# Kernel tuning notes

Hardware: AMD Instinct MI355X
Metric: run time of the kernel (lower is better)

## Reference

```python
import jax, jax.numpy as jnp
import numpy as np

K = 1024   # number of NNLS components (theta_1 is K x K)
B = 8192   # batched frames / columns


def setup_inputs() -> dict:
    key = jax.random.key(0)
    k1, k2, k3, k4 = jax.random.split(key, 4)
    # theta_1 = I - AtA / ||AtA||_F  -> near-identity contraction; emulate with
    # identity minus a small random symmetric-ish perturbation.
    pert = jax.random.normal(k1, (K, K), dtype=jnp.float32) * (1.0 / K)
    th1 = jnp.eye(K, dtype=jnp.float32) - pert
    Y = jax.random.uniform(k2, (K, B), dtype=jnp.float32)
    X_old = jax.random.uniform(k3, (K, B), dtype=jnp.float32)
    weight = jax.random.normal(k4, (K, B), dtype=jnp.float32) * 0.1  # theta_2 = Atb/n_AtA
    k = 2  # PGD iteration counter
    return {"th1": th1, "Y": Y, "X_old": X_old, "k": k, "weight": weight}


def reference(th1, Y, X_old, k, weight):
    # One projected-gradient-descent step of NNLS with Nesterov momentum:
    #   new_X = relu(th1 @ Y + weight)
    #   Y_new = new_X + (k-1)/(k+2) * (new_X - X_old)
    kf = jnp.float32(k)
    new_X = jax.nn.relu(jnp.matmul(th1, Y) + weight)          # [K, B]
    momentum = (kf - 1.0) / (kf + 2.0)
    Y_new = new_X + momentum * (new_X - X_old)                # [K, B]
    return (Y_new, new_X, k + 1, weight)
```

## Files before the change

### kernel.cpp

```cpp
#include <hip/hip_runtime.h>
#include <cstdint>


#define KDIM 1024
#define NDIM 8192
#define KB_ELEMS (1024UL * 8192UL)
#define LDA 40

typedef short short8 __attribute__((ext_vector_type(8)));
typedef float f32x4 __attribute__((ext_vector_type(4)));

struct __attribute__((aligned(4))) f4u { float x, y, z, w; };

__device__ __forceinline__ uint32_t pk2(float a, float b) {
  uint32_t ua = __builtin_bit_cast(uint32_t, a) + 0x8000u;
  uint32_t ub = __builtin_bit_cast(uint32_t, b) + 0x8000u;
  return (ua >> 16) | (ub & 0xFFFF0000u);
}

__global__ __launch_bounds__(512, 4) void nnls_gemm(
    const float* __restrict__ th1, const float* __restrict__ Y,
    const float* __restrict__ xold, const int* __restrict__ kin,
    const float* __restrict__ weight, float* __restrict__ out)
{
  __shared__ __align__(16) char smem[40960];
  unsigned short* As0 = (unsigned short*)smem;
  unsigned short* Bs0 = (unsigned short*)(smem + 10240);
  unsigned short* As1 = (unsigned short*)(smem + 20480);
  unsigned short* Bs1 = (unsigned short*)(smem + 30720);

  const int tid  = threadIdx.x;
  const int lane = tid & 63;
  const int w    = tid >> 6;
  const int wm = w >> 1, wn = w & 1;
  const int quad = lane >> 4, nl = lane & 15;

  const int m0 = blockIdx.y * 128;
  const int n0 = blockIdx.x * 128;

  const int ar = tid >> 3;
  const int ac = tid & 7;
  const float* abase = th1 + (size_t)(m0 + ar) * KDIM + ac * 4;

  const int bn = tid & 127;
  const int bk = (tid >> 7) * 8;
  const float* ybase = Y + (size_t)bk * NDIM + n0 + bn;

  float4 ab[2];
  float  yb[8];
  ab[0] = *(const float4*)(abase);
  ab[1] = *(const float4*)(abase + (size_t)64 * KDIM);
#pragma unroll
  for (int r = 0; r < 8; ++r) yb[r] = ybase[(size_t)r * NDIM];

  f32x4 acc[2][4] = {};

#pragma unroll 2
  for (int kt = 0; kt < 32; ++kt) {
    unsigned short* Asp = (kt & 1) ? As1 : As0;
    unsigned short* Bsp = (kt & 1) ? Bs1 : Bs0;

    {
      uint2 d0; d0.x = pk2(ab[0].x, ab[0].y); d0.y = pk2(ab[0].z, ab[0].w);
      *(uint2*)&Asp[ar * LDA + ac * 4] = d0;
      uint2 d1; d1.x = pk2(ab[1].x, ab[1].y); d1.y = pk2(ab[1].z, ab[1].w);
      *(uint2*)&Asp[(ar + 64) * LDA + ac * 4] = d1;
      uint4 e;
      e.x = pk2(yb[0], yb[1]); e.y = pk2(yb[2], yb[3]);
      e.z = pk2(yb[4], yb[5]); e.w = pk2(yb[6], yb[7]);
      *(uint4*)&Bsp[bn * LDA + bk] = e;
    }
    __syncthreads();

    if (kt < 31) {
      const float* an = abase + (kt + 1) * 32;
      ab[0] = *(const float4*)(an);
      ab[1] = *(const float4*)(an + (size_t)64 * KDIM);
      const float* yn = ybase + (size_t)((kt + 1) * 32) * NDIM;
#pragma unroll
      for (int r = 0; r < 8; ++r) yb[r] = yn[(size_t)r * NDIM];
    }

    short8 af[2], bf[4];
#pragma unroll
    for (int i = 0; i < 2; ++i)
      af[i] = *(const short8*)&Asp[(wm * 32 + i * 16 + nl) * LDA + quad * 8];
#pragma unroll
    for (int j = 0; j < 4; ++j)
      bf[j] = *(const short8*)&Bsp[(wn * 64 + j * 16 + nl) * LDA + quad * 8];
#pragma unroll
    for (int i = 0; i < 2; ++i)
#pragma unroll
      for (int j = 0; j < 4; ++j)
        acc[i][j] = __builtin_amdgcn_mfma_f32_16x16x32_bf16(af[i], bf[j], acc[i][j], 0, 0, 0);
  }
  __syncthreads();

  const float kf  = (float)kin[0];
  const float mom = (kf - 1.0f) / (kf + 2.0f);
  float* ep = (float*)smem + w * 1088;
  const int u  = lane >> 4;
  const int mc = lane & 15;

#pragma unroll
  for (int i = 0; i < 2; ++i) {
#pragma unroll
    for (int j = 0; j < 4; ++j)
#pragma unroll
      for (int r = 0; r < 4; ++r)
        ep[(quad * 4 + r) * 68 + (j * 16 + nl)] = acc[i][j][r];

    const int mgb = m0 + wm * 32 + i * 16;
#pragma unroll
    for (int t = 0; t < 4; ++t) {
      const int row = t * 4 + u;
      const float4 cv = *(const float4*)&ep[row * 68 + mc * 4];
      const int ng = n0 + wn * 64 + mc * 4;
      const size_t idx = (size_t)(mgb + row) * NDIM + ng;
      const float4 wv = *(const float4*)&weight[idx];
      const float4 xo = *(const float4*)&xold[idx];
      float4 nx, yn;
      nx.x = fmaxf(cv.x + wv.x, 0.0f); nx.y = fmaxf(cv.y + wv.y, 0.0f);
      nx.z = fmaxf(cv.z + wv.z, 0.0f); nx.w = fmaxf(cv.w + wv.w, 0.0f);
      yn.x = nx.x + mom * (nx.x - xo.x); yn.y = nx.y + mom * (nx.y - xo.y);
      yn.z = nx.z + mom * (nx.z - xo.z); yn.w = nx.w + mom * (nx.w - xo.w);
      *(float4*)&out[idx] = yn;
      *(float4*)&out[KB_ELEMS + idx] = nx;
      f4u s; s.x = wv.x; s.y = wv.y; s.z = wv.z; s.w = wv.w;
      *(f4u*)&out[2 * KB_ELEMS + 1 + idx] = s;
    }
  }

  if (blockIdx.x == 0 && blockIdx.y == 0 && tid == 0)
    out[2 * KB_ELEMS] = (float)(kin[0] + 1);
}

extern "C" void kernel_launch(void* const* d_in, const int* in_sizes, int n_in,
                              void* d_out, int out_size, void* d_ws, size_t ws_size,
                              hipStream_t stream) {
  const float* th1  = (const float*)d_in[0];
  const float* Y    = (const float*)d_in[1];
  const float* xold = (const float*)d_in[2];
  const int*   kin  = (const int*)d_in[3];
  const float* wgt  = (const float*)d_in[4];
  float* out = (float*)d_out;

  dim3 grid(NDIM / 128, KDIM / 128);
  nnls_gemm<<<grid, 512, 0, stream>>>(th1, Y, xold, kin, wgt, out);
}
```

Measured before the change: 221.0 us.

## Pre-convert operands to bf16 tiled layout and stream via direct LDS loads

```diff
diff --git a/kernel.cpp b/kernel.cpp
--- a/kernel.cpp
+++ b/kernel.cpp
@@ -5,7 +5,9 @@
 #define KDIM 1024
 #define NDIM 8192
 #define KB_ELEMS (1024UL * 8192UL)
-#define LDA 40
+#define YT_BYTES (8192UL * 1024UL * 2UL)
+#define AB_BYTES (1024UL * 1024UL * 2UL)
+#define WS_NEED (YT_BYTES + AB_BYTES)
 
 typedef short short8 __attribute__((ext_vector_type(8)));
 typedef float f32x4 __attribute__((ext_vector_type(4)));
@@ -18,7 +20,155 @@
   return (ua >> 16) | (ub & 0xFFFF0000u);
 }
 
-__global__ __launch_bounds__(512, 4) void nnls_gemm(
+__device__ __forceinline__ void ldsload16(const void* g, void* l) {
+  __builtin_amdgcn_global_load_lds(
+      (const __attribute__((address_space(1))) uint32_t*)g,
+      (__attribute__((address_space(3))) uint32_t*)l, 16, 0, 0);
+}
+
+__global__ __launch_bounds__(256) void nnls_conv(
+    const float* __restrict__ th1, const float* __restrict__ Y,
+    char* __restrict__ ws)
+{
+  unsigned short* yt  = (unsigned short*)ws;
+  unsigned short* abf = (unsigned short*)(ws + YT_BYTES);
+  const int tid = threadIdx.x;
+  if (blockIdx.x < 1024) {
+    const int kt = blockIdx.x >> 5;
+    const int nb = blockIdx.x & 31;
+    const int k0 = kt * 32, n0 = nb * 256;
+    __shared__ float t[32][260];
+#pragma unroll
+    for (int it = 0; it < 8; ++it) {
+      const int r = it * 4 + (tid >> 6);
+      const float4 v = *(const float4*)&Y[(size_t)(k0 + r) * NDIM + n0 + (tid & 63) * 4];
+      *(float4*)&t[r][(tid & 63) * 4] = v;
+    }
+    __syncthreads();
+    const int n = tid;
+    __attribute__((aligned(16))) uint32_t o[16];
+#pragma unroll
+    for (int r2 = 0; r2 < 16; ++r2) o[r2] = pk2(t[2 * r2][n], t[2 * r2 + 1][n]);
+    uint32_t* dst = (uint32_t*)&yt[((size_t)kt * NDIM + (n0 + n)) * 32];
+#pragma unroll
+    for (int q = 0; q < 4; ++q) *(uint4*)&dst[q * 4] = *(uint4*)&o[q * 4];
+  } else {
+    const int id = (blockIdx.x - 1024) * 256 + tid;
+    const int m = id >> 5, kt = id & 31;
+    const float4* s4 = (const float4*)(th1 + (size_t)m * KDIM + kt * 32);
+    __attribute__((aligned(16))) uint32_t o[16];
+#pragma unroll
+    for (int q = 0; q < 8; ++q) {
+      const float4 v = s4[q];
+      o[2 * q]     = pk2(v.x, v.y);
+      o[2 * q + 1] = pk2(v.z, v.w);
+    }
+    uint32_t* dst = (uint32_t*)&abf[((size_t)kt * KDIM + m) * 32];
+#pragma unroll
+    for (int q = 0; q < 4; ++q) *(uint4*)&dst[q * 4] = *(uint4*)&o[q * 4];
+  }
+}
+
+__global__ __launch_bounds__(256, 4) void nnls_gemm2(
+    const char* __restrict__ ws, const float* __restrict__ xold,
+    const int* __restrict__ kin, const float* __restrict__ weight,
+    float* __restrict__ out)
+{
+  const char* yt = ws;
+  const char* ab = ws + YT_BYTES;
+  __shared__ __align__(16) char smem[24576];
+
+  const int tid  = threadIdx.x;
+  const int lane = tid & 63;
+  const int w    = tid >> 6;
+  const int wm = w >> 1, wn = w & 1;
+  const int quad = lane >> 4, nl = lane & 15;
+
+  const int m0 = blockIdx.y * 128;
+  const int n0 = blockIdx.x * 64;
+
+  const char* ag = ab + (size_t)m0 * 64 + w * 2048 + lane * 16;
+  const char* bg = yt + (size_t)n0 * 64 + w * 1024 + lane * 16;
+
+  f32x4 acc[4][2] = {};
+
+  {
+    char* buf = smem;
+    ldsload16(ag,        buf + w * 2048);
+    ldsload16(ag + 1024, buf + w * 2048 + 1024);
+    ldsload16(bg,        buf + 8192 + w * 1024);
+  }
+  __syncthreads();
+
+#pragma unroll 2
+  for (int kt = 0; kt < 32; ++kt) {
+    char* cur = smem + (kt & 1) * 12288;
+    char* nxt = smem + ((kt & 1) ^ 1) * 12288;
+    if (kt < 31) {
+      const char* a2 = ag + (size_t)(kt + 1) * 65536;
+      const char* b2 = bg + (size_t)(kt + 1) * 524288;
+      ldsload16(a2,        nxt + w * 2048);
+      ldsload16(a2 + 1024, nxt + w * 2048 + 1024);
+      ldsload16(b2,        nxt + 8192 + w * 1024);
+    }
+    const unsigned short* Asp = (const unsigned short*)cur;
+    const unsigned short* Bsp = (const unsigned short*)(cur + 8192);
+    short8 af[4], bf[2];
+#pragma unroll
+    for (int i = 0; i < 4; ++i)
+      af[i] = *(const short8*)&Asp[(wm * 64 + i * 16 + nl) * 32 + quad * 8];
+#pragma unroll
+    for (int j = 0; j < 2; ++j)
+      bf[j] = *(const short8*)&Bsp[(wn * 32 + j * 16 + nl) * 32 + quad * 8];
+#pragma unroll
+    for (int i = 0; i < 4; ++i)
+#pragma unroll
+      for (int j = 0; j < 2; ++j)
+        acc[i][j] = __builtin_amdgcn_mfma_f32_16x16x32_bf16(af[i], bf[j], acc[i][j], 0, 0, 0);
+    __syncthreads();
+  }
+
+  const float kf  = (float)kin[0];
+  const float mom = (kf - 1.0f) / (kf + 2.0f);
+  float* ep = (float*)(smem + w * 2304);
+  const int rl = lane >> 3;
+  const int cq = lane & 7;
+
+#pragma unroll
+  for (int i = 0; i < 4; ++i) {
+#pragma unroll
+    for (int j = 0; j < 2; ++j)
+#pragma unroll
+      for (int r = 0; r < 4; ++r)
+        ep[(quad * 4 + r) * 36 + (j * 16 + nl)] = acc[i][j][r];
+
+    const int mgb = m0 + wm * 64 + i * 16;
+#pragma unroll
+    for (int t = 0; t < 2; ++t) {
+      const int row = t * 8 + rl;
+      const float4 cv = *(const float4*)&ep[row * 36 + cq * 4];
+      const int ng = n0 + wn * 32 + cq * 4;
+      const size_t idx = (size_t)(mgb + row) * NDIM + ng;
+      const float4 wv = *(const float4*)&weight[idx];
+      const float4 xo = *(const float4*)&xold[idx];
+      float4 nx, yn;
+      nx.x = fmaxf(cv.x + wv.x, 0.0f); nx.y = fmaxf(cv.y + wv.y, 0.0f);
+      nx.z = fmaxf(cv.z + wv.z, 0.0f); nx.w = fmaxf(cv.w + wv.w, 0.0f);
+      yn.x = nx.x + mom * (nx.x - xo.x); yn.y = nx.y + mom * (nx.y - xo.y);
+      yn.z = nx.z + mom * (nx.z - xo.z); yn.w = nx.w + mom * (nx.w - xo.w);
+      *(float4*)&out[idx] = yn;
+      *(float4*)&out[KB_ELEMS + idx] = nx;
+      f4u s; s.x = wv.x; s.y = wv.y; s.z = wv.z; s.w = wv.w;
+      *(f4u*)&out[2 * KB_ELEMS + 1 + idx] = s;
+    }
+  }
+
+  if (blockIdx.x == 0 && blockIdx.y == 0 && tid == 0)
+    out[2 * KB_ELEMS] = (float)(kin[0] + 1);
+}
+
+#define LDA 40
+__global__ __launch_bounds__(512, 4) void nnls_gemm_v1(
     const float* __restrict__ th1, const float* __restrict__ Y,
     const float* __restrict__ xold, const int* __restrict__ kin,
     const float* __restrict__ weight, float* __restrict__ out)
@@ -34,22 +184,19 @@
   const int w    = tid >> 6;
   const int wm = w >> 1, wn = w & 1;
   const int quad = lane >> 4, nl = lane & 15;
-
   const int m0 = blockIdx.y * 128;
   const int n0 = blockIdx.x * 128;
-
   const int ar = tid >> 3;
   const int ac = tid & 7;
   const float* abase = th1 + (size_t)(m0 + ar) * KDIM + ac * 4;
-
   const int bn = tid & 127;
   const int bk = (tid >> 7) * 8;
   const float* ybase = Y + (size_t)bk * NDIM + n0 + bn;
 
-  float4 ab[2];
+  float4 abv[2];
   float  yb[8];
-  ab[0] = *(const float4*)(abase);
-  ab[1] = *(const float4*)(abase + (size_t)64 * KDIM);
+  abv[0] = *(const float4*)(abase);
+  abv[1] = *(const float4*)(abase + (size_t)64 * KDIM);
 #pragma unroll
   for (int r = 0; r < 8; ++r) yb[r] = ybase[(size_t)r * NDIM];
 
@@ -59,11 +206,10 @@
   for (int kt = 0; kt < 32; ++kt) {
     unsigned short* Asp = (kt & 1) ? As1 : As0;
     unsigned short* Bsp = (kt & 1) ? Bs1 : Bs0;
-
     {
-      uint2 d0; d0.x = pk2(ab[0].x, ab[0].y); d0.y = pk2(ab[0].z, ab[0].w);
+      uint2 d0; d0.x = pk2(abv[0].x, abv[0].y); d0.y = pk2(abv[0].z, abv[0].w);
       *(uint2*)&Asp[ar * LDA + ac * 4] = d0;
-      uint2 d1; d1.x = pk2(ab[1].x, ab[1].y); d1.y = pk2(ab[1].z, ab[1].w);
+      uint2 d1; d1.x = pk2(abv[1].x, abv[1].y); d1.y = pk2(abv[1].z, abv[1].w);
       *(uint2*)&Asp[(ar + 64) * LDA + ac * 4] = d1;
       uint4 e;
       e.x = pk2(yb[0], yb[1]); e.y = pk2(yb[2], yb[3]);
@@ -71,16 +217,14 @@
       *(uint4*)&Bsp[bn * LDA + bk] = e;
     }
     __syncthreads();
-
     if (kt < 31) {
       const float* an = abase + (kt + 1) * 32;
-      ab[0] = *(const float4*)(an);
-      ab[1] = *(const float4*)(an + (size_t)64 * KDIM);
+      abv[0] = *(const float4*)(an);
+      abv[1] = *(const float4*)(an + (size_t)64 * KDIM);
       const float* yn = ybase + (size_t)((kt + 1) * 32) * NDIM;
 #pragma unroll
       for (int r = 0; r < 8; ++r) yb[r] = yn[(size_t)r * NDIM];
     }
-
     short8 af[2], bf[4];
 #pragma unroll
     for (int i = 0; i < 2; ++i)
@@ -93,6 +237,7 @@
 #pragma unroll
       for (int j = 0; j < 4; ++j)
         acc[i][j] = __builtin_amdgcn_mfma_f32_16x16x32_bf16(af[i], bf[j], acc[i][j], 0, 0, 0);
+    __syncthreads();
   }
   __syncthreads();
 
@@ -101,7 +246,6 @@
   float* ep = (float*)smem + w * 1088;
   const int u  = lane >> 4;
   const int mc = lane & 15;
-
 #pragma unroll
   for (int i = 0; i < 2; ++i) {
 #pragma unroll
@@ -109,7 +253,6 @@
 #pragma unroll
       for (int r = 0; r < 4; ++r)
         ep[(quad * 4 + r) * 68 + (j * 16 + nl)] = acc[i][j][r];
-
     const int mgb = m0 + wm * 32 + i * 16;
 #pragma unroll
     for (int t = 0; t < 4; ++t) {
@@ -130,7 +273,6 @@
       *(f4u*)&out[2 * KB_ELEMS + 1 + idx] = s;
     }
   }
-
   if (blockIdx.x == 0 && blockIdx.y == 0 && tid == 0)
     out[2 * KB_ELEMS] = (float)(kin[0] + 1);
 }
@@ -145,6 +287,12 @@
   const float* wgt  = (const float*)d_in[4];
   float* out = (float*)d_out;
 
-  dim3 grid(NDIM / 128, KDIM / 128);
-  nnls_gemm<<<grid, 512, 0, stream>>>(th1, Y, xold, kin, wgt, out);
-}
+  if (d_ws != nullptr && ws_size >= WS_NEED) {
+    nnls_conv<<<1152, 256, 0, stream>>>(th1, Y, (char*)d_ws);
+    nnls_gemm2<<<dim3(NDIM / 64, KDIM / 128), 256, 0, stream>>>(
+        (const char*)d_ws, xold, kin, wgt, out);
+  } else {
+    nnls_gemm_v1<<<dim3(NDIM / 128, KDIM / 128), 512, 0, stream>>>(
+        th1, Y, xold, kin, wgt, out);
+  }
+}
```

Measured after the change: 226.5 us. 2.5% more time.
